# Performance work log

Measured on AMD Instinct MI355X. Metric: run time of the kernel, lower is better.

The kernel has to match this reference:

```python
import jax, jax.numpy as jnp
import numpy as np

# Module configuration (matches init_kwargs)
B = 128           # batch
C = 21            # in_channels
L = 2048          # in_features
W = 32            # window_size
S = 8             # strides
O = 16            # out_channels
EPS = 1e-6
M = int((L - W) / S - EPS)      # number of regularly-strided windows (251)
NW = M + 1                       # total windows incl. clamped last one (252)
NK = O * NW                      # 4032
# window start positions: j*S for j<M, last window clamped to L-W
STARTS = np.concatenate([np.arange(M) * S, np.array([L - W])]).astype(np.int32)


def setup_inputs() -> dict:
    key = jax.random.key(0)
    kx, kw = jax.random.split(key)
    x = jax.random.normal(kx, (B, C, L), dtype=jnp.float32)
    # original init: 2*(rand-0.5)/sqrt(W*C), uniform in [-1,1]/sqrt(W*C)
    weight = (2.0 * (jax.random.uniform(kw, (NK, W * C), dtype=jnp.float32) - 0.5)
              / np.sqrt(W * C).astype(np.float32))
    return {"x": x, "weight": weight}


def reference(x, weight):
    # im2col gather implied by the sparse fbank: patches[b,c,j,w] = x[b,c,starts[j]+w]
    idx = jnp.asarray(STARTS)[:, None] + jnp.arange(W)[None, :]   # (NW, W)
    patches = x[:, :, idx]                                        # (B, C, NW, W)
    # weight rows are n = j*O + o, columns laid out k*W + w (channel-major)
    w4 = weight.reshape(NW, O, C, W)                              # (NW, O, C, W)
    # h[b, j*O+o] = sum_{c,w} patches[b,c,j,w] * w4[j,o,c,w]
    h = jnp.einsum('bcjw,jocw->bjo', patches, w4)                 # (B, NW, O)
    return h.reshape(B, NK)
```

## Files before the change

### kernel.cpp

```cpp
#include <hip/hip_runtime.h>
#include <hip/hip_bf16.h>

#define Bb   128
#define Cc   21
#define Ll   2048
#define Ss   8
#define Oo   16
#define NWw  252
#define NKk  4032
#define Kk   672

typedef __attribute__((ext_vector_type(8))) short  short8;
typedef __attribute__((ext_vector_type(4))) float  f32x4;

static __device__ __forceinline__ unsigned short f2bf(float f) {
    union { __hip_bfloat16 h; unsigned short u; } cv;
    cv.h = __float2bfloat16(f);
    return cv.u;
}

static __device__ __forceinline__ short8 cvt8(const float4 a0, const float4 a1) {
    short8 a;
    a[0] = (short)f2bf(a0.x); a[1] = (short)f2bf(a0.y);
    a[2] = (short)f2bf(a0.z); a[3] = (short)f2bf(a0.w);
    a[4] = (short)f2bf(a1.x); a[5] = (short)f2bf(a1.y);
    a[6] = (short)f2bf(a1.z); a[7] = (short)f2bf(a1.w);
    return a;
}

__global__ __launch_bounds__(256, 4)
void fb_fwd(const float* __restrict__ x, const float* __restrict__ w,
            float* __restrict__ out) {
    const int bid = blockIdx.x;
    const int r   = bid & 7;
    const int t2  = bid >> 3;
    const int j   = r * 32 + (t2 >> 1);
    const int bh  = t2 & 1;
    if (j >= NWw) return;

    const int s    = (j < NWw - 1) ? j * Ss : (Ll - 32);
    const int tid  = threadIdx.x;
    const int lane = tid & 63;
    const int wv   = tid >> 6;
    const int col  = lane & 15;
    const int quad = lane >> 4;

    const float* xrow = x + ((size_t)(bh * 64 + wv * 16 + col) * Cc) * Ll
                          + s + quad * 8;
    const float* wrow = w + (size_t)j * Oo * Kk + (size_t)col * Kk + quad * 8;

    f32x4 acc = {0.f, 0.f, 0.f, 0.f};
#pragma unroll
    for (int c = 0; c < Cc; ++c) {
        const float4 a0 = *(const float4*)(xrow + (size_t)c * Ll);
        const float4 a1 = *(const float4*)(xrow + (size_t)c * Ll + 4);
        const float4 b0 = *(const float4*)(wrow + c * 32);
        const float4 b1 = *(const float4*)(wrow + c * 32 + 4);
        acc = __builtin_amdgcn_mfma_f32_16x16x32_bf16(
            cvt8(a0, a1), cvt8(b0, b1), acc, 0, 0, 0);
    }

    const int rbase = bh * 64 + wv * 16 + quad * 4;
    float* op = out + (size_t)rbase * NKk + j * 16 + col;
#pragma unroll
    for (int rr = 0; rr < 4; ++rr)
        op[(size_t)rr * NKk] = acc[rr];
}

extern "C" void kernel_launch(void* const* d_in, const int* in_sizes, int n_in,
                              void* d_out, int out_size, void* d_ws, size_t ws_size,
                              hipStream_t stream) {
    const float* x = (const float*)d_in[0];
    const float* w = (const float*)d_in[1];
    float* out = (float*)d_out;
    fb_fwd<<<dim3(512), dim3(256), 0, stream>>>(x, w, out);
}
```

Measured before the change: 88.71 us.

## Stage overlapping x windows in LDS as bf16 and share across eight windows

Each block now loads a contiguous span of x (16 batches × 21 channels × 88 columns) once, converts it to bf16, and stores it in shared memory. Eight overlapping windows are then computed from that tile, two per wave. Before, every window re-read its overlapping 32-element slices of x from global memory and converted them in registers. The grid shrinks from 512 to 256 blocks, which means fewer blocks and less parallelism on a many-CU GPU. The change also adds a syncthreads, a serialized staging phase, and about 64 KB of LDS per block, which limits occupancy.

```diff
diff --git a/kernel.cpp b/kernel.cpp
--- a/kernel.cpp
+++ b/kernel.cpp
@@ -9,6 +9,7 @@
 #define NWw  252
 #define NKk  4032
 #define Kk   672
+#define XP   96
 
 typedef __attribute__((ext_vector_type(8))) short  short8;
 typedef __attribute__((ext_vector_type(4))) float  f32x4;
@@ -28,43 +29,63 @@
     return a;
 }
 
-__global__ __launch_bounds__(256, 4)
+__global__ __launch_bounds__(256, 2)
 void fb_fwd(const float* __restrict__ x, const float* __restrict__ w,
             float* __restrict__ out) {
+    __shared__ unsigned short xs[16 * Cc * XP];
+
     const int bid = blockIdx.x;
     const int r   = bid & 7;
-    const int t2  = bid >> 3;
-    const int j   = r * 32 + (t2 >> 1);
-    const int bh  = t2 & 1;
-    if (j >= NWw) return;
+    const int t   = bid >> 3;
+    const int bt  = t & 7;
+    const int g   = t >> 3;
+    const int jb  = r * 32 + g * 8;
+    const int c_lo = r * 256 + g * 64;
+    const int c_hi = (c_lo + 88 < Ll) ? c_lo + 88 : Ll;
+    const int tid  = threadIdx.x;
 
-    const int s    = (j < NWw - 1) ? j * Ss : (Ll - 32);
-    const int tid  = threadIdx.x;
+    for (int i = tid; i < 336 * 22; i += 256) {
+        const int row = i / 22;
+        const int f4  = i - row * 22;
+        const int col = c_lo + f4 * 4;
+        if (col < c_hi) {
+            const float4 v =
+                *(const float4*)(x + ((size_t)(bt * 336 + row)) * Ll + col);
+            *(ushort4*)&xs[row * XP + f4 * 4] =
+                make_ushort4(f2bf(v.x), f2bf(v.y), f2bf(v.z), f2bf(v.w));
+        }
+    }
+    __syncthreads();
+
     const int lane = tid & 63;
     const int wv   = tid >> 6;
     const int col  = lane & 15;
     const int quad = lane >> 4;
 
-    const float* xrow = x + ((size_t)(bh * 64 + wv * 16 + col) * Cc) * Ll
-                          + s + quad * 8;
-    const float* wrow = w + (size_t)j * Oo * Kk + (size_t)col * Kk + quad * 8;
+    for (int wloc = 0; wloc < 2; ++wloc) {
+        const int j = jb + wv * 2 + wloc;
+        if (j >= NWw) continue;
+        const int s    = (j < NWw - 1) ? j * Ss : (Ll - 32);
+        const int soff = s - c_lo;
 
-    f32x4 acc = {0.f, 0.f, 0.f, 0.f};
+        const float* wp = w + (size_t)j * Oo * Kk + (size_t)col * Kk + quad * 8;
+        const unsigned short* ap = &xs[col * (Cc * XP) + soff + quad * 8];
+
+        f32x4 acc = {0.f, 0.f, 0.f, 0.f};
 #pragma unroll
-    for (int c = 0; c < Cc; ++c) {
-        const float4 a0 = *(const float4*)(xrow + (size_t)c * Ll);
-        const float4 a1 = *(const float4*)(xrow + (size_t)c * Ll + 4);
-        const float4 b0 = *(const float4*)(wrow + c * 32);
-        const float4 b1 = *(const float4*)(wrow + c * 32 + 4);
-        acc = __builtin_amdgcn_mfma_f32_16x16x32_bf16(
-            cvt8(a0, a1), cvt8(b0, b1), acc, 0, 0, 0);
+        for (int cc = 0; cc < Cc; ++cc) {
+            const float4 b0 = *(const float4*)(wp + cc * 32);
+            const float4 b1 = *(const float4*)(wp + cc * 32 + 4);
+            const short8 a  = *(const short8*)(ap + cc * XP);
+            acc = __builtin_amdgcn_mfma_f32_16x16x32_bf16(
+                a, cvt8(b0, b1), acc, 0, 0, 0);
+        }
+
+        float* op = out + (size_t)(bt * 16 + quad * 4) * NKk + j * 16 + col;
+#pragma unroll
+        for (int rr = 0; rr < 4; ++rr)
+            op[(size_t)rr * NKk] = acc[rr];
     }
-
-    const int rbase = bh * 64 + wv * 16 + quad * 4;
-    float* op = out + (size_t)rbase * NKk + j * 16 + col;
-#pragma unroll
-    for (int rr = 0; rr < 4; ++rr)
-        op[(size_t)rr * NKk] = acc[rr];
 }
 
 extern "C" void kernel_launch(void* const* d_in, const int* in_sizes, int n_in,
@@ -73,5 +94,5 @@
     const float* x = (const float*)d_in[0];
     const float* w = (const float*)d_in[1];
     float* out = (float*)d_out;
-    fb_fwd<<<dim3(512), dim3(256), 0, stream>>>(x, w, out);
+    fb_fwd<<<dim3(256), dim3(256), 0, stream>>>(x, w, out);
 }
```

After: 89.37 us. About the same (+0.7%).
